# Performance work log

Measured on AMD Instinct MI355X. Metric: run time of the kernel, lower is better.

The kernel has to match this reference:

```python
import jax, jax.numpy as jnp
import numpy as np

EMBED_DIM = 1024
NUM_HEADS = 16
HEAD_DIM = EMBED_DIM // NUM_HEADS


def setup_inputs() -> dict:
    key = jax.random.key(0)
    ks = jax.random.split(key, 9)
    D = EMBED_DIM
    s = 1.0 / np.sqrt(D)
    x = jax.random.normal(ks[0], (2, 2048, D), dtype=jnp.float32)
    Wq = jax.random.uniform(ks[1], (D, D), jnp.float32, -s, s)
    bq = jax.random.uniform(ks[2], (D,), jnp.float32, -s, s)
    Wk = jax.random.uniform(ks[3], (D, D), jnp.float32, -s, s)
    bk = jax.random.uniform(ks[4], (D,), jnp.float32, -s, s)
    Wv = jax.random.uniform(ks[5], (D, D), jnp.float32, -s, s)
    bv = jax.random.uniform(ks[6], (D,), jnp.float32, -s, s)
    Wo = jax.random.uniform(ks[7], (D, D), jnp.float32, -s, s)
    bo = jax.random.uniform(ks[8], (D,), jnp.float32, -s, s)
    return {"x": x, "Wq": Wq, "bq": bq, "Wk": Wk, "bk": bk,
            "Wv": Wv, "bv": bv, "Wo": Wo, "bo": bo}


def reference(x, Wq, bq, Wk, bk, Wv, bv, Wo, bo):
    B, N, D = x.shape
    H, Dh = NUM_HEADS, HEAD_DIM
    # QKV projections (weights stored as [in, out] = torch W.T)
    q = (x @ Wq + bq).reshape(B, N, H, Dh).transpose(0, 2, 1, 3)  # b h n d
    k = (x @ Wk + bk).reshape(B, N, H, Dh).transpose(0, 2, 1, 3)
    v = (x @ Wv + bv).reshape(B, N, H, Dh).transpose(0, 2, 1, 3)
    # NOTE: original divides by head_dim (not sqrt(head_dim))
    scores = jnp.einsum('bhnd,bhmd->bhnm', q, k) / Dh
    probs = jax.nn.softmax(scores, axis=-1)
    out = jnp.einsum('bhnm,bhmd->bhnd', probs, v)  # b h n d
    out = out.transpose(0, 2, 1, 3).reshape(B, N, D)
    return out @ Wo + bo
```

## Files before the change

kernel.cpp:

```cpp
#include <hip/hip_runtime.h>
#include <hip/hip_bf16.h>

constexpr int EMBED = 1024;
constexpr int NHEAD = 16;
constexpr int HDIM  = 64;
constexpr int BATCH = 2;
constexpr int SEQ   = 2048;
constexpr int MROWS = BATCH * SEQ;
constexpr int NKB   = EMBED / 32;
constexpr int NT    = SEQ / 64;

typedef __attribute__((ext_vector_type(8)))  short          bf8;
typedef __attribute__((ext_vector_type(8)))  unsigned short us8;
typedef __attribute__((ext_vector_type(16))) float          f32x16;
typedef __attribute__((ext_vector_type(2)))  int            i32x2;

__device__ __forceinline__ unsigned short f2bf(float f) {
  unsigned u = __float_as_uint(f);
  u += 0x7fffu + ((u >> 16) & 1u);
  return (unsigned short)(u >> 16);
}
__device__ __forceinline__ void async16(const void* g, void* l) {
  __builtin_amdgcn_global_load_lds(
      (const __attribute__((address_space(1))) unsigned int*)g,
      (__attribute__((address_space(3))) unsigned int*)l, 16, 0, 0);
}
__device__ __forceinline__ i32x2 swap32(int a, int b) {
  return __builtin_amdgcn_permlane32_swap(a, b, false, false);
}
__device__ __forceinline__ unsigned cvt2(float a, float b) {
  union { __hip_bfloat162 bb; unsigned u; } cv;
  cv.bb = __float22bfloat162_rn(float2{a, b});
  return cv.u;
}
__device__ __forceinline__ void bar_pre() {
  __builtin_amdgcn_s_barrier();
  __builtin_amdgcn_sched_barrier(0);
}
__device__ __forceinline__ void bar_post() {
  __builtin_amdgcn_sched_barrier(0);
  __builtin_amdgcn_s_barrier();
}

__global__ __launch_bounds__(256) void pack_all2_k(
    const float* __restrict__ x,
    const float* __restrict__ W0, const float* __restrict__ W1,
    const float* __restrict__ W2, const float* __restrict__ W3,
    char* __restrict__ Xp, char* __restrict__ Wpk)
{
  __shared__ float LDSf[8 * 1032];
  const int blk = blockIdx.x;
  const int tid = threadIdx.x;
  if (blk < 2048) {
    int sid = blk * 256 + tid;
    int s = sid & 7, t = (sid >> 3) & 31, u = sid >> 8;
    int c = s ^ (u & 7);
    int par = c >> 2, kq = c & 3;
    const float* src = x + (size_t)(2 * u + par) * EMBED + t * 32 + kq * 8;
    us8 o;
    #pragma unroll
    for (int e = 0; e < 8; ++e) o[e] = f2bf(src[e]);
    *(us8*)(Xp + ((size_t)sid << 4)) = o;
  } else {
    const int bb = blk - 2048;
    const int y = bb >> 7, r = bb & 127, t = r >> 2, q = r & 3;
    const float* W = (y == 0) ? W0 : (y == 1) ? W1 : (y == 2) ? W2 : W3;
    char* op = Wpk + ((size_t)y << 21);
    #pragma unroll
    for (int it = 0; it < 8; ++it) {
      int f4 = it * 256 + tid;
      int row = f4 >> 8, col4 = (f4 & 255) << 2;
      float4 v = *(const float4*)(W + (size_t)(t * 32 + q * 8 + row) * EMBED + col4);
      *(float4*)(&LDSf[row * 1032 + col4]) = v;
    }
    __syncthreads();
    #pragma unroll
    for (int it = 0; it < 4; ++it) {
      int sid2 = it * 256 + tid;
      int u = sid2 >> 1, par = sid2 & 1;
      int s = ((par << 2) | q) ^ (u & 7);
      us8 o;
      #pragma unroll
      for (int e = 0; e < 8; ++e) o[e] = f2bf(LDSf[e * 1032 + 2 * u + par]);
      *(us8*)(op + (((size_t)(u << 8) + (t << 3) + s) << 4)) = o;
    }
  }
}

__global__ __launch_bounds__(256) void gemm_qkv_fused_k(
    const char* __restrict__ Apk, const char* __restrict__ Wpk,
    const float* __restrict__ B0, const float* __restrict__ B1, const float* __restrict__ B2,
    unsigned short* __restrict__ Qbf, unsigned short* __restrict__ Kbf,
    unsigned short* __restrict__ Vt)
{
  __shared__ __align__(16) char lds[57344];

  const int tid  = threadIdx.x;
  const int lane = tid & 63;
  const int wid  = tid >> 6;
  const int ln31 = lane & 31, lhalf = lane >> 5;

  const int bid = blockIdx.x;
  const int swz = (bid & 7) * 64 + (bid >> 3);
  const int rp  = swz >> 3, cb = swz & 7;

  const int M0 = rp * 64, N0 = cb * 128;
  const int U0 = rp * 32, V0 = cb * 64;

  const char* ab = Apk + ((size_t)(U0 + (tid >> 3)) << 12) + ((tid & 7) << 4);
  const int la = tid * 16;
  const char* wb[2]; int lw[2];
  #pragma unroll
  for (int i = 0; i < 2; ++i) {
    int idx = i * 256 + tid;
    wb[i] = Wpk + ((size_t)(V0 + (idx >> 3)) << 12) + ((idx & 7) << 4);
    lw[i] = 4096 + i * 4096 + tid * 16;
  }

  f32x16 acc[3][2];
  #pragma unroll
  for (int z = 0; z < 3; ++z)
    #pragma unroll
    for (int mi = 0; mi < 2; ++mi)
      #pragma unroll
      for (int q = 0; q < 16; ++q) acc[z][mi][q] = 0.f;

  async16(ab, lds + la);
  #pragma unroll
  for (int z = 0; z < 3; ++z)
    #pragma unroll
    for (int i = 0; i < 2; ++i)
      async16(wb[i] + ((size_t)z << 21), lds + z * 8192 + lw[i]);

  for (int t = 0; t < NKB; ++t) {
    const int c = t & 1;
    if (t + 1 < NKB) {
      const int off = (t + 1) << 7;
      async16(ab + off, lds + (c ^ 1) * 28672 + la);
      #pragma unroll
      for (int z = 0; z < 3; ++z)
        #pragma unroll
        for (int i = 0; i < 2; ++i)
          async16(wb[i] + ((size_t)z << 21) + off,
                  lds + (c ^ 1) * 28672 + z * 8192 + lw[i]);
      asm volatile("s_waitcnt vmcnt(7)" ::: "memory");
    } else {
      asm volatile("s_waitcnt vmcnt(0)" ::: "memory");
    }
    bar_pre();
    const char* Ab = lds + c * 28672;
    const char* Wb = Ab + 4096;
    #pragma unroll
    for (int kb = 0; kb < 2; ++kb) {
      const int kq = (kb << 1) | lhalf;
      bf8 a[2];
      #pragma unroll
      for (int mi = 0; mi < 2; ++mi) {
        int m = mi * 32 + ln31;
        int u = m >> 1;
        int s = (((m & 1) << 2) | kq) ^ (u & 7);
        a[mi] = *(const bf8*)(Ab + u * 128 + s * 16);
      }
      const int n = wid * 32 + ln31;
      const int un = n >> 1;
      const int sn = (((n & 1) << 2) | kq) ^ (un & 7);
      #pragma unroll
      for (int z = 0; z < 3; ++z) {
        bf8 b = *(const bf8*)(Wb + z * 8192 + un * 128 + sn * 16);
        acc[z][0] = __builtin_amdgcn_mfma_f32_32x32x16_bf16(a[0], b, acc[z][0], 0, 0, 0);
        acc[z][1] = __builtin_amdgcn_mfma_f32_32x32x16_bf16(a[1], b, acc[z][1], 0, 0, 0);
      }
    }
    bar_post();
  }

  const int col = N0 + wid * 32 + ln31;
  #pragma unroll
  for (int z = 0; z < 2; ++z) {
    unsigned short* Cb = (z == 0) ? Qbf : Kbf;
    const float* Bv = (z == 0) ? B0 : B1;
    const float sc = (z == 0) ? (1.44269504088896f / 64.0f) : 1.0f;
    float bb = Bv[col];
    #pragma unroll
    for (int mi = 0; mi < 2; ++mi)
      #pragma unroll
      for (int r = 0; r < 16; ++r) {
        int row = M0 + mi * 32 + (r & 3) + ((r >> 2) << 3) + (lhalf << 2);
        Cb[(size_t)row * EMBED + col] = f2bf((acc[z][mi][r] + bb) * sc);
      }
  }
  {
    const int tile = (M0 & 2047) >> 6;
    const int bb   = M0 >> 11;
    const int hh = col >> 6, dl = col & 63;
    const float bv = B2[col];
    size_t base2 = (((size_t)(bb * 16 + hh)) << 17) + ((size_t)tile << 12) + (dl << 6);
    unsigned pkq[2][4][2];
    #pragma unroll
    for (int mi = 0; mi < 2; ++mi)
      #pragma unroll
      for (int rg = 0; rg < 4; ++rg) {
        pkq[mi][rg][0] = cvt2(acc[2][mi][4 * rg + 0] + bv, acc[2][mi][4 * rg + 1] + bv);
        pkq[mi][rg][1] = cvt2(acc[2][mi][4 * rg + 2] + bv, acc[2][mi][4 * rg + 3] + bv);
      }
    #pragma unroll
    for (int gk = 0; gk < 8; ++gk) {
      const int mi = gk >> 2, rg = gk & 3;
      i32x2 e0 = swap32((int)pkq[mi][rg][0], (int)pkq[mi][rg][0]);
      i32x2 e1 = swap32((int)pkq[mi][rg][1], (int)pkq[mi][rg][1]);
      int g = gk ^ (dl & 7);
      if ((g >> 2) == lhalf) {
        union { unsigned u[4]; us8 v; } o;
        o.u[0] = (unsigned)e0[0]; o.u[1] = (unsigned)e1[0];
        o.u[2] = (unsigned)e0[1]; o.u[3] = (unsigned)e1[1];
        *(us8*)(Vt + base2 + (g << 3)) = o.v;
      }
    }
  }
}

__global__ __launch_bounds__(256) void gemm_out_bf16_k(
    const char* __restrict__ Apk, const char* __restrict__ Wpk,
    const float* __restrict__ Bv, float* __restrict__ Cf)
{
  __shared__ __align__(16) char lds[49152];

  const int tid  = threadIdx.x;
  const int lane = tid & 63;
  const int wid  = tid >> 6;
  const int ln31 = lane & 31, lhalf = lane >> 5;

  const int bid = blockIdx.x;
  const int swz = (bid & 7) * 64 + (bid >> 3);
  const int rp  = swz >> 3, cb = swz & 7;

  const int M0 = rp * 64, N0 = cb * 128;
  const int U0 = rp * 32, V0 = cb * 64;

  const char* ab[2]; int la[2];
  #pragma unroll
  for (int i = 0; i < 2; ++i) {
    int idx = i * 256 + tid;
    int ul = idx >> 4, tt = (idx >> 3) & 1, sl = idx & 7;
    ab[i] = Apk + ((size_t)(U0 + ul) << 12) + (tt << 7) + (sl << 4);
    la[i] = i * 4096 + tid * 16;
  }
  const char* wb[4]; int lw[4];
  #pragma unroll
  for (int j = 0; j < 4; ++j) {
    int idx = j * 256 + tid;
    int ul = idx >> 4, tt = (idx >> 3) & 1, sl = idx & 7;
    wb[j] = Wpk + ((size_t)(V0 + ul) << 12) + (tt << 7) + (sl << 4);
    lw[j] = 8192 + j * 4096 + tid * 16;
  }

  f32x16 acc[2];
  #pragma unroll
  for (int mi = 0; mi < 2; ++mi)
    #pragma unroll
    for (int q = 0; q < 16; ++q) acc[mi][q] = 0.f;

  #pragma unroll
  for (int i = 0; i < 2; ++i) async16(ab[i], lds + la[i]);
  #pragma unroll
  for (int j = 0; j < 4; ++j) async16(wb[j], lds + lw[j]);

  for (int T = 0; T < NKB / 2; ++T) {
    const int c = T & 1;
    if (T + 1 < NKB / 2) {
      const int off = (T + 1) << 8;
      #pragma unroll
      for (int i = 0; i < 2; ++i) async16(ab[i] + off, lds + (c ^ 1) * 24576 + la[i]);
      #pragma unroll
      for (int j = 0; j < 4; ++j) async16(wb[j] + off, lds + (c ^ 1) * 24576 + lw[j]);
      asm volatile("s_waitcnt vmcnt(6)" ::: "memory");
    } else {
      asm volatile("s_waitcnt vmcnt(0)" ::: "memory");
    }
    bar_pre();
    const char* Ab = lds + c * 24576;
    const char* Wb = Ab + 8192;
    #pragma unroll
    for (int tt = 0; tt < 2; ++tt) {
      #pragma unroll
      for (int kb = 0; kb < 2; ++kb) {
        const int kq = (kb << 1) | lhalf;
        bf8 a[2];
        #pragma unroll
        for (int mi = 0; mi < 2; ++mi) {
          int m = mi * 32 + ln31;
          int u = m >> 1;
          int s = (((m & 1) << 2) | kq) ^ (u & 7);
          a[mi] = *(const bf8*)(Ab + u * 256 + tt * 128 + s * 16);
        }
        const int n = wid * 32 + ln31;
        const int un = n >> 1;
        const int sn = (((n & 1) << 2) | kq) ^ (un & 7);
        bf8 b = *(const bf8*)(Wb + un * 256 + tt * 128 + sn * 16);
        acc[0] = __builtin_amdgcn_mfma_f32_32x32x16_bf16(a[0], b, acc[0], 0, 0, 0);
        acc[1] = __builtin_amdgcn_mfma_f32_32x32x16_bf16(a[1], b, acc[1], 0, 0, 0);
      }
    }
    bar_post();
  }

  const int col = N0 + wid * 32 + ln31;
  const float bb = Bv[col];
  #pragma unroll
  for (int mi = 0; mi < 2; ++mi)
    #pragma unroll
    for (int r = 0; r < 16; ++r) {
      int row = M0 + mi * 32 + (r & 3) + ((r >> 2) << 3) + (lhalf << 2);
      Cf[(size_t)row * EMBED + col] = acc[mi][r] + bb;
    }
}

__global__ __launch_bounds__(512) void attn_mfma_k(
    const unsigned short* __restrict__ Qb, const unsigned short* __restrict__ Kb,
    const char* __restrict__ Vt, char* __restrict__ A2)
{
  __shared__ __align__(16) char lds[65536];

  const int bid = blockIdx.x;
  const int swz = (bid & 7) * 64 + (bid >> 3);
  const int qt = swz & 15, h = (swz >> 4) & 15, b = swz >> 8;

  const int tid  = threadIdx.x;
  const int kw   = tid >> 8;
  const int tidg = tid & 255;
  const int lane = tid & 63;
  const int qw   = (tid >> 6) & 3;
  const int ln31 = lane & 31, lh = lane >> 5;
  const int l7   = ln31 & 7;

  const int q0 = qt * 128;
  const int sbase = kw * 32768;
  const int T0 = kw * 16;

  bf8 qf[4];
  {
    const size_t qoff = (size_t)(b * SEQ + q0 + qw * 32 + ln31) * EMBED + h * HDIM;
    #pragma unroll
    for (int kd = 0; kd < 4; ++kd)
      qf[kd] = *(const bf8*)(Qb + qoff + (2 * kd + lh) * 8);
  }

  const unsigned short* ksrc[2];
  const char* vtb = Vt + ((size_t)(b * 16 + h) << 18);
  int ldoff[2];
  #pragma unroll
  for (int i = 0; i < 2; ++i) {
    int idx = i * 256 + tidg;
    int r = idx >> 3, s7 = idx & 7;
    int un = s7 ^ (r & 7);
    ksrc[i] = Kb + (size_t)(b * SEQ + r) * EMBED + h * HDIM + un * 8;
    ldoff[i] = i * 4096 + (tidg >> 6) * 1024;
  }

  #pragma unroll
  for (int i = 0; i < 2; ++i) {
    async16(ksrc[i] + (size_t)(T0 * 64) * EMBED, lds + sbase + ldoff[i]);
    async16(vtb + (T0 << 13) + ((i * 256 + tidg) << 4), lds + sbase + 8192 + ldoff[i]);
  }

  const bf8 ones = {0x3F80, 0x3F80, 0x3F80, 0x3F80, 0x3F80, 0x3F80, 0x3F80, 0x3F80};
  f32x16 z16;
  #pragma unroll
  for (int r = 0; r < 16; ++r) z16[r] = 0.f;

  f32x16 oacc[2], oacc3;
  #pragma unroll
  for (int df = 0; df < 2; ++df)
    #pragma unroll
    for (int r = 0; r < 16; ++r) oacc[df][r] = 0.f;
  oacc3 = z16;

  for (int it = 0; it < NT / 2; ++it) {
    const int c = it & 1;
    if (it + 1 < NT / 2) {
      const int tn = T0 + it + 1;
      #pragma unroll
      for (int i = 0; i < 2; ++i) {
        async16(ksrc[i] + (size_t)(tn * 64) * EMBED, lds + sbase + (c ^ 1) * 16384 + ldoff[i]);
        async16(vtb + (tn << 13) + ((i * 256 + tidg) << 4),
                lds + sbase + (c ^ 1) * 16384 + 8192 + ldoff[i]);
      }
      asm volatile("s_waitcnt vmcnt(4)" ::: "memory");
    } else {
      asm volatile("s_waitcnt vmcnt(0)" ::: "memory");
    }
    bar_pre();
    const char* Kbuf = lds + sbase + c * 16384;
    const char* Vbuf = Kbuf + 8192;

    f32x16 sacc[2];
    __builtin_amdgcn_s_setprio(1);
    #pragma unroll
    for (int kf = 0; kf < 2; ++kf) {
      bf8 ka0 = *(const bf8*)(Kbuf + (32 * kf + ln31) * 128 + ((lh ^ l7) << 4));
      sacc[kf] = __builtin_amdgcn_mfma_f32_32x32x16_bf16(ka0, qf[0], z16, 0, 0, 0);
      #pragma unroll
      for (int kd = 1; kd < 4; ++kd) {
        bf8 ka = *(const bf8*)(Kbuf + (32 * kf + ln31) * 128 + (((2 * kd + lh) ^ l7) << 4));
        sacc[kf] = __builtin_amdgcn_mfma_f32_32x32x16_bf16(ka, qf[kd], sacc[kf], 0, 0, 0);
      }
    }
    __builtin_amdgcn_s_setprio(0);

    unsigned pk[2][8];
    #pragma unroll
    for (int g = 0; g < 4; ++g)
      #pragma unroll
      for (int j = 0; j < 2; ++j)
        pk[0][2 * g + j] = cvt2(__builtin_amdgcn_exp2f(sacc[0][4 * g + 2 * j]),
                                __builtin_amdgcn_exp2f(sacc[0][4 * g + 2 * j + 1]));
    __builtin_amdgcn_s_setprio(1);
    #pragma unroll
    for (int kb = 0; kb < 2; ++kb) {
      const int b4 = (kb & 1) * 4;
      i32x2 r02 = swap32((int)pk[0][b4 + 0], (int)pk[0][b4 + 2]);
      i32x2 r13 = swap32((int)pk[0][b4 + 1], (int)pk[0][b4 + 3]);
      union { unsigned u[4]; bf8 v; } pf;
      pf.u[0] = (unsigned)r02[0]; pf.u[1] = (unsigned)r13[0];
      pf.u[2] = (unsigned)r02[1]; pf.u[3] = (unsigned)r13[1];
      #pragma unroll
      for (int df = 0; df < 2; ++df) {
        bf8 va = *(const bf8*)(Vbuf + (32 * df + ln31) * 128 + (((2 * kb + lh) ^ l7) << 4));
        oacc[df] = __builtin_amdgcn_mfma_f32_32x32x16_bf16(va, pf.v, oacc[df], 0, 0, 0);
      }
      oacc3 = __builtin_amdgcn_mfma_f32_32x32x16_bf16(ones, pf.v, oacc3, 0, 0, 0);
    }
    __builtin_amdgcn_s_setprio(0);
    #pragma unroll
    for (int g = 0; g < 4; ++g)
      #pragma unroll
      for (int j = 0; j < 2; ++j)
        pk[1][2 * g + j] = cvt2(__builtin_amdgcn_exp2f(sacc[1][4 * g + 2 * j]),
                                __builtin_amdgcn_exp2f(sacc[1][4 * g + 2 * j + 1]));
    __builtin_amdgcn_s_setprio(1);
    #pragma unroll
    for (int kb = 2; kb < 4; ++kb) {
      const int b4 = (kb & 1) * 4;
      i32x2 r02 = swap32((int)pk[1][b4 + 0], (int)pk[1][b4 + 2]);
      i32x2 r13 = swap32((int)pk[1][b4 + 1], (int)pk[1][b4 + 3]);
      union { unsigned u[4]; bf8 v; } pf;
      pf.u[0] = (unsigned)r02[0]; pf.u[1] = (unsigned)r13[0];
      pf.u[2] = (unsigned)r02[1]; pf.u[3] = (unsigned)r13[1];
      #pragma unroll
      for (int df = 0; df < 2; ++df) {
        bf8 va = *(const bf8*)(Vbuf + (32 * df + ln31) * 128 + (((2 * kb + lh) ^ l7) << 4));
        oacc[df] = __builtin_amdgcn_mfma_f32_32x32x16_bf16(va, pf.v, oacc[df], 0, 0, 0);
      }
      oacc3 = __builtin_amdgcn_mfma_f32_32x32x16_bf16(ones, pf.v, oacc3, 0, 0, 0);
    }
    __builtin_amdgcn_s_setprio(0);
    bar_post();
  }

  float* ex = (float*)lds;
  const int slot = qw * 64 + lane;
  if (kw == 1) {
    #pragma unroll
    for (int df = 0; df < 2; ++df)
      #pragma unroll
      for (int r = 0; r < 16; ++r)
        ex[slot * 34 + df * 16 + r] = oacc[df][r];
    ex[slot * 34 + 32] = oacc3[0];
  }
  __syncthreads();
  if (kw == 1) return;

  #pragma unroll
  for (int df = 0; df < 2; ++df)
    #pragma unroll
    for (int r = 0; r < 16; ++r)
      oacc[df][r] += ex[slot * 34 + df * 16 + r];
  const float ltot = oacc3[0] + ex[slot * 34 + 32];

  const float inv = 1.0f / ltot;
  float fl[8][4], fh[8][4];
  #pragma unroll
  for (int df = 0; df < 2; ++df)
    #pragma unroll
    for (int r = 0; r < 16; ++r) {
      float o = oacc[df][r] * inv;
      i32x2 rr = swap32(__float_as_int(o), __float_as_int(o));
      fl[df * 4 + (r >> 2)][r & 3] = __int_as_float(rr[0]);
      fh[df * 4 + (r >> 2)][r & 3] = __int_as_float(rr[1]);
    }

  const int row = b * SEQ + q0 + qw * 32 + ln31;
  const int u = row >> 1, par = row & 1;
  #pragma unroll
  for (int g = 0; g < 8; ++g) {
    us8 hi;
    #pragma unroll
    for (int e = 0; e < 8; ++e) {
      float f = (e < 4) ? fl[g][e] : fh[g][e - 4];
      hi[e] = f2bf(f);
    }
    int t_blk = 2 * h + (g >> 2), kq = g & 3;
    size_t ub = ((size_t)(u * 32 + t_blk)) << 7;
    int s = ((par << 2) | kq) ^ (u & 7);
    *(us8*)(A2 + ub + (s << 4)) = hi;
  }
}

extern "C" void kernel_launch(void* const* d_in, const int* in_sizes, int n_in,
                              void* d_out, int out_size, void* d_ws, size_t ws_size,
                              hipStream_t stream)
{
  const float* x  = (const float*)d_in[0];
  const float* Wq = (const float*)d_in[1];
  const float* bq = (const float*)d_in[2];
  const float* Wk = (const float*)d_in[3];
  const float* bk = (const float*)d_in[4];
  const float* Wv = (const float*)d_in[5];
  const float* bv = (const float*)d_in[6];
  const float* Wo = (const float*)d_in[7];
  const float* bo = (const float*)d_in[8];
  float* out = (float*)d_out;

  char* wsb = (char*)d_ws;
  char*           Xp  = wsb;
  char*           Wpk = wsb + ((size_t)8  << 20);
  unsigned short* Qbf = (unsigned short*)(wsb + ((size_t)16 << 20));
  unsigned short* Kbf = (unsigned short*)(wsb + ((size_t)24 << 20));
  unsigned short* Vtp = (unsigned short*)(wsb + ((size_t)32 << 20));
  char*           A2  = wsb + ((size_t)40 << 20);

  pack_all2_k<<<dim3(2560), dim3(256), 0, stream>>>(
      x, Wq, Wk, Wv, Wo, Xp, Wpk);

  gemm_qkv_fused_k<<<dim3(512), dim3(256), 0, stream>>>(
      Xp, Wpk, bq, bk, bv, Qbf, Kbf, Vtp);

  attn_mfma_k<<<dim3(512), dim3(512), 0, stream>>>(
      Qbf, Kbf, (const char*)Vtp, A2);

  gemm_out_bf16_k<<<dim3(512), dim3(256), 0, stream>>>(
      A2, Wpk + ((size_t)3 << 21), bo, out);
}
```

Measured before the change: 110.3 us.

## Drop split-KV in attention; use 8 query waves per block over full sequence

The attention kernel previously split each 128-query tile's key range across two groups of four waves and merged partial outputs and row sums through LDS at the end. It now gives each block 256 queries across eight waves, each covering the full key sequence, which halves the grid to 256 blocks and removes the cross-group reduction. K/V tiles are loaded once per block and shared by all eight waves, so each K/V tile is reused across more queries and the LDS footprint halves. The trade-off is half as many blocks, which on a chip with many CUs can leave some CUs idle, and a serial key loop twice as long.

```diff
diff --git a/kernel.cpp b/kernel.cpp
--- a/kernel.cpp
+++ b/kernel.cpp
@@ -319,23 +319,19 @@
     const unsigned short* __restrict__ Qb, const unsigned short* __restrict__ Kb,
     const char* __restrict__ Vt, char* __restrict__ A2)
 {
-  __shared__ __align__(16) char lds[65536];
+  __shared__ __align__(16) char lds[32768];
 
   const int bid = blockIdx.x;
-  const int swz = (bid & 7) * 64 + (bid >> 3);
-  const int qt = swz & 15, h = (swz >> 4) & 15, b = swz >> 8;
+  const int swz = (bid & 7) * 32 + (bid >> 3);
+  const int qt = swz & 7, h = (swz >> 3) & 15, b = swz >> 7;
 
   const int tid  = threadIdx.x;
-  const int kw   = tid >> 8;
-  const int tidg = tid & 255;
   const int lane = tid & 63;
-  const int qw   = (tid >> 6) & 3;
+  const int qw   = tid >> 6;
   const int ln31 = lane & 31, lh = lane >> 5;
   const int l7   = ln31 & 7;
 
-  const int q0 = qt * 128;
-  const int sbase = kw * 32768;
-  const int T0 = kw * 16;
+  const int q0 = qt * 256;
 
   bf8 qf[4];
   {
@@ -345,23 +341,17 @@
       qf[kd] = *(const bf8*)(Qb + qoff + (2 * kd + lh) * 8);
   }
 
-  const unsigned short* ksrc[2];
+  const unsigned short* ksrc;
+  {
+    int r = tid >> 3, s7 = tid & 7;
+    int un = s7 ^ (r & 7);
+    ksrc = Kb + (size_t)(b * SEQ + r) * EMBED + h * HDIM + un * 8;
+  }
   const char* vtb = Vt + ((size_t)(b * 16 + h) << 18);
-  int ldoff[2];
-  #pragma unroll
-  for (int i = 0; i < 2; ++i) {
-    int idx = i * 256 + tidg;
-    int r = idx >> 3, s7 = idx & 7;
-    int un = s7 ^ (r & 7);
-    ksrc[i] = Kb + (size_t)(b * SEQ + r) * EMBED + h * HDIM + un * 8;
-    ldoff[i] = i * 4096 + (tidg >> 6) * 1024;
-  }
-
-  #pragma unroll
-  for (int i = 0; i < 2; ++i) {
-    async16(ksrc[i] + (size_t)(T0 * 64) * EMBED, lds + sbase + ldoff[i]);
-    async16(vtb + (T0 << 13) + ((i * 256 + tidg) << 4), lds + sbase + 8192 + ldoff[i]);
-  }
+  const int lk = tid * 16;
+
+  async16(ksrc, lds + lk);
+  async16(vtb + lk, lds + 8192 + lk);
 
   const bf8 ones = {0x3F80, 0x3F80, 0x3F80, 0x3F80, 0x3F80, 0x3F80, 0x3F80, 0x3F80};
   f32x16 z16;
@@ -375,22 +365,17 @@
     for (int r = 0; r < 16; ++r) oacc[df][r] = 0.f;
   oacc3 = z16;
 
-  for (int it = 0; it < NT / 2; ++it) {
-    const int c = it & 1;
-    if (it + 1 < NT / 2) {
-      const int tn = T0 + it + 1;
-      #pragma unroll
-      for (int i = 0; i < 2; ++i) {
-        async16(ksrc[i] + (size_t)(tn * 64) * EMBED, lds + sbase + (c ^ 1) * 16384 + ldoff[i]);
-        async16(vtb + (tn << 13) + ((i * 256 + tidg) << 4),
-                lds + sbase + (c ^ 1) * 16384 + 8192 + ldoff[i]);
-      }
-      asm volatile("s_waitcnt vmcnt(4)" ::: "memory");
+  for (int t = 0; t < NT; ++t) {
+    const int c = t & 1;
+    if (t + 1 < NT) {
+      async16(ksrc + (size_t)((t + 1) * 64) * EMBED, lds + (c ^ 1) * 16384 + lk);
+      async16(vtb + ((t + 1) << 13) + lk, lds + (c ^ 1) * 16384 + 8192 + lk);
+      asm volatile("s_waitcnt vmcnt(2)" ::: "memory");
     } else {
       asm volatile("s_waitcnt vmcnt(0)" ::: "memory");
     }
     bar_pre();
-    const char* Kbuf = lds + sbase + c * 16384;
+    const char* Kbuf = lds + c * 16384;
     const char* Vbuf = Kbuf + 8192;
 
     f32x16 sacc[2];
@@ -457,27 +442,7 @@
     bar_post();
   }
 
-  float* ex = (float*)lds;
-  const int slot = qw * 64 + lane;
-  if (kw == 1) {
-    #pragma unroll
-    for (int df = 0; df < 2; ++df)
-      #pragma unroll
-      for (int r = 0; r < 16; ++r)
-        ex[slot * 34 + df * 16 + r] = oacc[df][r];
-    ex[slot * 34 + 32] = oacc3[0];
-  }
-  __syncthreads();
-  if (kw == 1) return;
-
-  #pragma unroll
-  for (int df = 0; df < 2; ++df)
-    #pragma unroll
-    for (int r = 0; r < 16; ++r)
-      oacc[df][r] += ex[slot * 34 + df * 16 + r];
-  const float ltot = oacc3[0] + ex[slot * 34 + 32];
-
-  const float inv = 1.0f / ltot;
+  const float inv = 1.0f / oacc3[0];
   float fl[8][4], fh[8][4];
   #pragma unroll
   for (int df = 0; df < 2; ++df)
@@ -535,7 +500,7 @@
   gemm_qkv_fused_k<<<dim3(512), dim3(256), 0, stream>>>(
       Xp, Wpk, bq, bk, bv, Qbf, Kbf, Vtp);
 
-  attn_mfma_k<<<dim3(512), dim3(512), 0, stream>>>(
+  attn_mfma_k<<<dim3(256), dim3(512), 0, stream>>>(
       Qbf, Kbf, (const char*)Vtp, A2);
 
   gemm_out_bf16_k<<<dim3(512), dim3(256), 0, stream>>>(
```

New measurement: 112.2 us. About the same (+1.8%).
